# Optimization experiments

Measured on AMD Instinct MI355X. Metric: run time of the kernel, lower is better.

## Reference

```python
import jax, jax.numpy as jnp
import numpy as np
import math

N = 1024
C = 128
H = 4
HD = C // H  # 32
HID = C // 2  # geom_mlp hidden


def setup_inputs() -> dict:
    key = jax.random.key(0)
    ks = jax.random.split(key, 12)
    s = 0.02
    return {
        "x": jax.random.normal(ks[0], (N, C), jnp.float32),
        "y": jax.random.normal(ks[1], (N, C), jnp.float32),
        "pos": jax.random.normal(ks[2], (N, 3), jnp.float32),
        "Wq": jax.random.normal(ks[3], (C, C), jnp.float32) * s,
        "bq": jnp.zeros((C,), jnp.float32),
        "Wk": jax.random.normal(ks[4], (C, C), jnp.float32) * s,
        "bk": jnp.zeros((C,), jnp.float32),
        "Wv": jax.random.normal(ks[5], (C, C), jnp.float32) * s,
        "bv": jnp.zeros((C,), jnp.float32),
        "W1": jax.random.normal(ks[6], (3, HID), jnp.float32) * s,
        "b1": jnp.zeros((HID,), jnp.float32),
        "W2": jax.random.normal(ks[7], (HID, C), jnp.float32) * s,
        "b2": jnp.zeros((C,), jnp.float32),
    }


def _safe_norm(sq):
    # sqrt with zero (sub)gradient at 0, matching torch.norm behavior
    pos_mask = sq > 0
    return jnp.where(pos_mask, jnp.sqrt(jnp.where(pos_mask, sq, 1.0)), 0.0)


def reference(x, y, pos, Wq, bq, Wk, bk, Wv, bv, W1, b1, W2, b2):
    # pairwise geometry
    pos_diff = pos[:, None, :] - pos[None, :, :]          # [N, N, 3]
    dist = _safe_norm(jnp.sum(pos_diff * pos_diff, -1))   # [N, N]
    geom = jax.nn.relu(pos_diff @ W1 + b1) @ W2 + b2      # [N, N, C]
    geom = geom.reshape(N, N, H, HD)                      # per-head split

    q = (x @ Wq + bq).reshape(N, H, HD)
    k = (y @ Wk + bk).reshape(N, H, HD)
    v = (y @ Wv + bv).reshape(N, H, HD)

    attn = jnp.einsum("ihd,jhd->hij", q, k) / math.sqrt(HD)  # [H, N, N]
    geom_attn = jnp.einsum("ihd,ijhd->hij", q, geom)         # [H, N, N]
    scores = attn + geom_attn - dist[None, :, :]
    p = jax.nn.softmax(scores, axis=-1)
    out = jnp.einsum("hij,jhd->ihd", p, v).reshape(N, C)     # [N, C]
    return out
```

## Files before the change

kernel.cpp:

```cpp
#include <hip/hip_runtime.h>
#include <math.h>


typedef float v2f __attribute__((ext_vector_type(2)));
typedef float v4f __attribute__((ext_vector_type(4)));

#define L2E 1.4426950408889634f
#define RSL (0.17677669529663687f * L2E)

static __device__ __forceinline__ float dot4(float4 a, float4 b) {
  return a.x*b.x + a.y*b.y + a.z*b.z + a.w*b.w;
}
static __device__ __forceinline__ v2f fma2(v2f a, v2f b, v2f c) {
  return __builtin_elementwise_fma(a, b, c);
}
static __device__ __forceinline__ v4f fma4s(float s, v4f b, v4f c) {
  v4f sv = {s, s, s, s};
  return __builtin_elementwise_fma(sv, b, c);
}
static __device__ __forceinline__ unsigned int bfr(float f) {
  unsigned int b = __float_as_uint(f);
  return (b + 0x7fffu + ((b >> 16) & 1u)) >> 16;
}
static __device__ __forceinline__ unsigned int pack2(float lo, float hi) {
  return bfr(lo) | (bfr(hi) << 16);
}
static __device__ __forceinline__ v2f unpk(unsigned int a) {
  v2f r;
  r.x = __uint_as_float(a << 16);
  r.y = __uint_as_float(a & 0xffff0000u);
  return r;
}

__global__ __launch_bounds__(384) void k_pre(
    const float* __restrict__ x, const float* __restrict__ y, const float* __restrict__ pos,
    const float* __restrict__ Wq, const float* __restrict__ bq,
    const float* __restrict__ Wk, const float* __restrict__ bk,
    const float* __restrict__ Wv, const float* __restrict__ bv,
    const float* __restrict__ W1, const float* __restrict__ b1,
    const float* __restrict__ W2, const float* __restrict__ b2,
    float* __restrict__ q, float* __restrict__ v,
    unsigned int* __restrict__ kTb, unsigned int* __restrict__ uTb,
    float* __restrict__ sA, float* __restrict__ pos4w)
{
  __shared__ float xs[256], ys[256], qs[256];
  __shared__ __align__(16) float4 W2S[64*33];

  const int t  = threadIdx.x;
  const int n0 = blockIdx.x * 2;

  if (t < 256) { xs[t] = x[n0*128 + t]; ys[t] = y[n0*128 + t]; }
  {
    const float4* w2g = (const float4*)W2;
    #pragma unroll
    for (int r = 0; r < 6; ++r) {
      const int e = t + 384*r;
      if (e < 2048) W2S[(e>>5)*33 + (e&31)] = w2g[e];
    }
  }
  __syncthreads();

  {
    const int c   = t & 127;
    const int mat = t >> 7;
    const float* W    = (mat == 0) ? Wq : (mat == 1 ? Wk : Wv);
    const float* S    = (mat == 0) ? xs : ys;
    const float* bias = (mat == 0) ? bq : (mat == 1 ? bk : bv);
    float a0 = 0.f, a1 = 0.f;
    #pragma unroll 8
    for (int d = 0; d < 128; ++d) {
      const float w_ = W[d*128 + c];
      a0 = fmaf(S[d],       w_, a0);
      a1 = fmaf(S[128 + d], w_, a1);
    }
    const float bb = bias[c];
    a0 += bb; a1 += bb;
    if (mat == 0) {
      q[n0*128 + c] = a0 * RSL; q[(n0+1)*128 + c] = a1 * RSL;
      qs[c] = a0; qs[128 + c] = a1;
    } else if (mat == 2) {
      v[n0*128 + c] = a0; v[(n0+1)*128 + c] = a1;
    } else {
      const float b0 = __shfl_xor(a0, 1);
      const float b1 = __shfl_xor(a1, 1);
      if ((c & 1) == 0) {
        const int idx = ((c>>2)*1024)*2 + ((c>>1)&1);
        kTb[idx + (n0  )*2] = pack2(a0, b0);
        kTb[idx + (n0+1)*2] = pack2(a1, b1);
      }
    }
  }
  __syncthreads();

  if (t < 256) {
    const int m = t & 63, h = t >> 6;
    const float4* qs4 = (const float4*)qs;
    #pragma unroll
    for (int ii = 0; ii < 2; ++ii) {
      float acc = 0.f;
      #pragma unroll
      for (int ch = 0; ch < 8; ++ch)
        acc += dot4(qs4[ii*32 + h*8 + ch], W2S[m*33 + h*8 + ch]);
      sA[(n0+ii)*328 + 8 + (m>>2)*20 + h*4 + (m&3)] = acc * L2E;
    }
    if (t < 8) {
      const int ii = t >> 2, h2 = t & 3;
      float ca = 0.f;
      #pragma unroll
      for (int d = 0; d < 32; ++d) ca = fmaf(qs[ii*128 + h2*32 + d], b2[h2*32 + d], ca);
      sA[(n0+ii)*328 + h2] = ca * L2E;
    } else if (t < 16) {
      const int tt = t-8, ii = tt>>2, cc = tt&3;
      sA[(n0+ii)*328 + 4 + cc] = (cc < 3) ? pos[(n0+ii)*3 + cc] * L2E : 0.f;
    } else if (t < 24) {
      const int tt = t-16, ii = tt>>2, cc = tt&3;
      pos4w[(n0+ii)*4 + cc] = (cc < 3) ? pos[(n0+ii)*3 + cc] * L2E : 0.f;
    }
  } else if (t < 320) {
    const int tt = t - 256, ii = tt >> 5, mp = tt & 31;
    const int m0 = mp * 2;
    float ua0 = 0.f, ua1 = 0.f;
    #pragma unroll
    for (int cc = 0; cc < 3; ++cc) {
      const float p = pos[(n0+ii)*3 + cc];
      ua0 = fmaf(p, W1[cc*64 + m0    ], ua0);
      ua1 = fmaf(p, W1[cc*64 + m0 + 1], ua1);
    }
    sA[(n0+ii)*328 + 8 + (m0>>2)*20 + 16 + (m0&3)    ] = ua0 + b1[m0];
    sA[(n0+ii)*328 + 8 + (m0>>2)*20 + 16 + (m0&3) + 1] = ua1 + b1[m0+1];
    uTb[((mp>>1)*1024 + (n0+ii))*2 + (mp&1)] = pack2(ua0, ua1);
  }
}

__global__ __launch_bounds__(1024, 8) void k_attn(
    const float* __restrict__ q, const float* __restrict__ v,
    const uint2* __restrict__ kTb, const uint2* __restrict__ uTb,
    const float* __restrict__ sA, const v4f* __restrict__ pos4,
    float* __restrict__ out)
{
  __shared__ __align__(16) float eL[16*544];
  __shared__ __align__(16) float rnum[8192];
  __shared__ float rden[128];

  const int t     = threadIdx.x;
  const int i0    = blockIdx.x * 2;
  const int w     = t >> 6;
  const int lane  = t & 63;
  const int c4    = lane & 31;
  const int rep   = lane >> 5;
  const int hh    = c4 >> 3;

  const int jb = w*64;
  const int j  = jb + lane;

  const float* sA0 = sA + i0*328;
  const float* sA1 = sA0 + 328;
  const float* q0  = q + i0*128;
  const float* q1  = q0 + 128;

  const float c00 = sA0[0], c01 = sA0[1], c02 = sA0[2], c03 = sA0[3];
  const float c10 = sA1[0], c11 = sA1[1], c12 = sA1[2], c13 = sA1[3];
  const float p0x = sA0[4], p0y = sA0[5], p0z = sA0[6];
  const float p1x = sA1[4], p1y = sA1[5], p1z = sA1[6];

  const v4f pj = pos4[j];
  const float d0x = p0x-pj.x, d0y = p0y-pj.y, d0z = p0z-pj.z;
  const float d1x = p1x-pj.x, d1y = p1y-pj.y, d1z = p1z-pj.z;
  const float dist0 = sqrtf(d0x*d0x + d0y*d0y + d0z*d0z);
  const float dist1 = sqrtf(d1x*d1x + d1y*d1y + d1z*d1z);

  v2f g0a={0.f,0.f}, g0b={0.f,0.f}, g0c={0.f,0.f}, g0d={0.f,0.f};
  v2f g1a={0.f,0.f}, g1b={0.f,0.f}, g1c={0.f,0.f}, g1d={0.f,0.f};
  #pragma unroll 4
  for (int mb = 0; mb < 16; ++mb) {
    const uint2 up_ = uTb[mb*1024 + j];
    const v2f uj01 = unpk(up_.x), uj23 = unpk(up_.y);
    const v2f z = {0.f, 0.f};
    {
      const float* ab = sA0 + 8 + mb*20;
      const v2f h01 = __builtin_elementwise_max(*(const v2f*)(ab+16) - uj01, z);
      const v2f h23 = __builtin_elementwise_max(*(const v2f*)(ab+18) - uj23, z);
      g0a = fma2(h01, *(const v2f*)(ab+ 0), g0a); g0a = fma2(h23, *(const v2f*)(ab+ 2), g0a);
      g0b = fma2(h01, *(const v2f*)(ab+ 4), g0b); g0b = fma2(h23, *(const v2f*)(ab+ 6), g0b);
      g0c = fma2(h01, *(const v2f*)(ab+ 8), g0c); g0c = fma2(h23, *(const v2f*)(ab+10), g0c);
      g0d = fma2(h01, *(const v2f*)(ab+12), g0d); g0d = fma2(h23, *(const v2f*)(ab+14), g0d);
    }
    {
      const float* ab = sA1 + 8 + mb*20;
      const v2f h01 = __builtin_elementwise_max(*(const v2f*)(ab+16) - uj01, z);
      const v2f h23 = __builtin_elementwise_max(*(const v2f*)(ab+18) - uj23, z);
      g1a = fma2(h01, *(const v2f*)(ab+ 0), g1a); g1a = fma2(h23, *(const v2f*)(ab+ 2), g1a);
      g1b = fma2(h01, *(const v2f*)(ab+ 4), g1b); g1b = fma2(h23, *(const v2f*)(ab+ 6), g1b);
      g1c = fma2(h01, *(const v2f*)(ab+ 8), g1c); g1c = fma2(h23, *(const v2f*)(ab+10), g1c);
      g1d = fma2(h01, *(const v2f*)(ab+12), g1d); g1d = fma2(h23, *(const v2f*)(ab+14), g1d);
    }
  }

  v2f s0a={0.f,0.f}, s0b={0.f,0.f}, s0c={0.f,0.f}, s0d={0.f,0.f};
  v2f s1a={0.f,0.f}, s1b={0.f,0.f}, s1c={0.f,0.f}, s1d={0.f,0.f};
  #pragma unroll 8
  for (int cb = 0; cb < 8; ++cb) {
    const uint2 kp0 = kTb[(cb     )*1024 + j];
    const uint2 kp1 = kTb[(cb +  8)*1024 + j];
    const uint2 kp2 = kTb[(cb + 16)*1024 + j];
    const uint2 kp3 = kTb[(cb + 24)*1024 + j];
    const v2f k0a = unpk(kp0.x), k0b = unpk(kp0.y);
    const v2f k1a = unpk(kp1.x), k1b = unpk(kp1.y);
    const v2f k2a = unpk(kp2.x), k2b = unpk(kp2.y);
    const v2f k3a = unpk(kp3.x), k3b = unpk(kp3.y);
    s0a = fma2(k0a, *(const v2f*)(q0 + cb*4      ), s0a); s0a = fma2(k0b, *(const v2f*)(q0 + cb*4 +  2), s0a);
    s0b = fma2(k1a, *(const v2f*)(q0 + cb*4 + 32 ), s0b); s0b = fma2(k1b, *(const v2f*)(q0 + cb*4 + 34), s0b);
    s0c = fma2(k2a, *(const v2f*)(q0 + cb*4 + 64 ), s0c); s0c = fma2(k2b, *(const v2f*)(q0 + cb*4 + 66), s0c);
    s0d = fma2(k3a, *(const v2f*)(q0 + cb*4 + 96 ), s0d); s0d = fma2(k3b, *(const v2f*)(q0 + cb*4 + 98), s0d);
    s1a = fma2(k0a, *(const v2f*)(q1 + cb*4      ), s1a); s1a = fma2(k0b, *(const v2f*)(q1 + cb*4 +  2), s1a);
    s1b = fma2(k1a, *(const v2f*)(q1 + cb*4 + 32 ), s1b); s1b = fma2(k1b, *(const v2f*)(q1 + cb*4 + 34), s1b);
    s1c = fma2(k2a, *(const v2f*)(q1 + cb*4 + 64 ), s1c); s1c = fma2(k2b, *(const v2f*)(q1 + cb*4 + 66), s1c);
    s1d = fma2(k3a, *(const v2f*)(q1 + cb*4 + 96 ), s1d); s1d = fma2(k3b, *(const v2f*)(q1 + cb*4 + 98), s1d);
  }

  float lsum[8];
  float* eW = &eL[w*544];
  {
    const v2f t0a = s0a + g0a, t0b = s0b + g0b, t0c = s0c + g0c, t0d = s0d + g0d;
    const float p0 = exp2f(t0a.x + t0a.y + (c00 - dist0));
    const float p1 = exp2f(t0b.x + t0b.y + (c01 - dist0));
    const float p2 = exp2f(t0c.x + t0c.y + (c02 - dist0));
    const float p3 = exp2f(t0d.x + t0d.y + (c03 - dist0));
    lsum[0] = p0; lsum[1] = p1; lsum[2] = p2; lsum[3] = p3;
    eW[      lane] = p0; eW[ 68 + lane] = p1; eW[136 + lane] = p2; eW[204 + lane] = p3;
    const v2f t1a = s1a + g1a, t1b = s1b + g1b, t1c = s1c + g1c, t1d = s1d + g1d;
    const float r0 = exp2f(t1a.x + t1a.y + (c10 - dist1));
    const float r1 = exp2f(t1b.x + t1b.y + (c11 - dist1));
    const float r2 = exp2f(t1c.x + t1c.y + (c12 - dist1));
    const float r3 = exp2f(t1d.x + t1d.y + (c13 - dist1));
    lsum[4] = r0; lsum[5] = r1; lsum[6] = r2; lsum[7] = r3;
    eW[272 + lane] = r0; eW[340 + lane] = r1; eW[408 + lane] = r2; eW[476 + lane] = r3;
  }
  __builtin_amdgcn_wave_barrier();

  v4f acc0 = {0.f,0.f,0.f,0.f};
  v4f acc1 = {0.f,0.f,0.f,0.f};
  {
    const v4f* er0 = (const v4f*)&eL[w*544 +  hh    *68 + rep*32];
    const v4f* er1 = (const v4f*)&eL[w*544 + (4+hh) *68 + rep*32];
    const v4f* vg = (const v4f*)(v + jb*128);
    const int vbase = rep*32*32 + c4;
    #pragma unroll 4
    for (int jj4 = 0; jj4 < 8; ++jj4) {
      const v4f e0 = er0[jj4];
      const v4f e1 = er1[jj4];
      const v4f va = vg[vbase + (jj4*4+0)*32];
      const v4f vb = vg[vbase + (jj4*4+1)*32];
      const v4f vc = vg[vbase + (jj4*4+2)*32];
      const v4f vd = vg[vbase + (jj4*4+3)*32];
      acc0 = fma4s(e0.x, va, acc0); acc1 = fma4s(e1.x, va, acc1);
      acc0 = fma4s(e0.y, vb, acc0); acc1 = fma4s(e1.y, vb, acc1);
      acc0 = fma4s(e0.z, vc, acc0); acc1 = fma4s(e1.z, vc, acc1);
      acc0 = fma4s(e0.w, vd, acc0); acc1 = fma4s(e1.w, vd, acc1);
    }
  }
  __builtin_amdgcn_wave_barrier();

  #pragma unroll
  for (int mm = 1; mm < 64; mm <<= 1) {
    #pragma unroll
    for (int r8 = 0; r8 < 8; ++r8) lsum[r8] += __shfl_xor(lsum[r8], mm);
  }
  ((v4f*)rnum)[((w*2+0)*2 + rep)*32 + c4] = acc0;
  ((v4f*)rnum)[((w*2+1)*2 + rep)*32 + c4] = acc1;
  if (lane == 0) {
    #pragma unroll
    for (int r8 = 0; r8 < 8; ++r8) rden[w*8 + r8] = lsum[r8];
  }
  __syncthreads();

  if (t < 256) {
    const int ii = t >> 7, c = t & 127;
    float num = 0.f, den = 0.f;
    #pragma unroll
    for (int ww = 0; ww < 16; ++ww) {
      num += rnum[((ww*2+ii)*2+0)*128 + c];
      num += rnum[((ww*2+ii)*2+1)*128 + c];
      den += rden[ww*8 + ii*4 + (c>>5)];
    }
    out[(i0+ii)*128 + c] = num / den;
  }
}

extern "C" void kernel_launch(void* const* d_in, const int* in_sizes, int n_in,
                              void* d_out, int out_size, void* d_ws, size_t ws_size,
                              hipStream_t stream) {
  const float* x   = (const float*)d_in[0];
  const float* y   = (const float*)d_in[1];
  const float* pos = (const float*)d_in[2];
  const float* Wq  = (const float*)d_in[3];
  const float* bq  = (const float*)d_in[4];
  const float* Wk  = (const float*)d_in[5];
  const float* bk  = (const float*)d_in[6];
  const float* Wv  = (const float*)d_in[7];
  const float* bv  = (const float*)d_in[8];
  const float* W1  = (const float*)d_in[9];
  const float* b1  = (const float*)d_in[10];
  const float* W2  = (const float*)d_in[11];
  const float* b2  = (const float*)d_in[12];

  float* ws = (float*)d_ws;
  float*        q    = ws;
  float*        v    = ws + 131072;
  unsigned int* kTb  = (unsigned int*)(ws + 262144);
  unsigned int* uTb  = (unsigned int*)(ws + 327680);
  float*        sA   = ws + 360448;
  float*        pos4 = ws + 696320;
  float*        out  = (float*)d_out;

  k_pre<<<dim3(512), dim3(384), 0, stream>>>(x, y, pos, Wq, bq, Wk, bk, Wv, bv,
                                             W1, b1, W2, b2,
                                             q, v, kTb, uTb, sA, pos4);
  k_attn<<<dim3(512), dim3(1024), 0, stream>>>(q, v, (const uint2*)kTb,
                                               (const uint2*)uTb, sA,
                                               (const v4f*)pos4, out);
}
```

Before: 116.9 us.

## Switch QK and PV products to packed fp16 dot2 with fp16 q/k/v storage

Stores scaled q, k and v as packed fp16 pairs (k moves from bf16 to fp16, v is laid out j-pair interleaved) and computes QK scores and the P·V accumulation with v_dot2 fp16 instructions instead of fp32 FMAs. The softmax numerators are rounded to fp16 so the row sums match the values used in the weighted sum. The denominator reduction is moved ahead of the PV loop. This halves the q/v global traffic and the FMA count, at the cost of fp16 range and precision risk on scores and exponentials.

```diff
diff --git a/kernel.cpp b/kernel.cpp
--- a/kernel.cpp
+++ b/kernel.cpp
@@ -1,9 +1,11 @@
 #include <hip/hip_runtime.h>
+#include <hip/hip_fp16.h>
 #include <math.h>
 
 
 typedef float v2f __attribute__((ext_vector_type(2)));
 typedef float v4f __attribute__((ext_vector_type(4)));
+typedef __fp16 h2f __attribute__((ext_vector_type(2)));
 
 #define L2E 1.4426950408889634f
 #define RSL (0.17677669529663687f * L2E)
@@ -13,10 +15,6 @@
 }
 static __device__ __forceinline__ v2f fma2(v2f a, v2f b, v2f c) {
   return __builtin_elementwise_fma(a, b, c);
-}
-static __device__ __forceinline__ v4f fma4s(float s, v4f b, v4f c) {
-  v4f sv = {s, s, s, s};
-  return __builtin_elementwise_fma(sv, b, c);
 }
 static __device__ __forceinline__ unsigned int bfr(float f) {
   unsigned int b = __float_as_uint(f);
@@ -30,6 +28,23 @@
   r.x = __uint_as_float(a << 16);
   r.y = __uint_as_float(a & 0xffff0000u);
   return r;
+}
+static __device__ __forceinline__ unsigned int pkh(float lo, float hi) {
+  h2f r = __builtin_amdgcn_cvt_pkrtz(lo, hi);
+  return __builtin_bit_cast(unsigned int, r);
+}
+static __device__ __forceinline__ unsigned int pkrn(float lo, float hi) {
+  unsigned int a = (unsigned int)__half_as_ushort(__float2half(lo));
+  unsigned int b = (unsigned int)__half_as_ushort(__float2half(hi));
+  return a | (b << 16);
+}
+static __device__ __forceinline__ float fdot2h(unsigned int a_, unsigned int b_, float acc) {
+  return __builtin_amdgcn_fdot2(__builtin_bit_cast(h2f, a_),
+                                __builtin_bit_cast(h2f, b_), acc, false);
+}
+static __device__ __forceinline__ float r2hf(float x) {
+  h2f t = __builtin_amdgcn_cvt_pkrtz(x, x);
+  return (float)t.x;
 }
 
 __global__ __launch_bounds__(384) void k_pre(
@@ -39,7 +54,7 @@
     const float* __restrict__ Wv, const float* __restrict__ bv,
     const float* __restrict__ W1, const float* __restrict__ b1,
     const float* __restrict__ W2, const float* __restrict__ b2,
-    float* __restrict__ q, float* __restrict__ v,
+    unsigned int* __restrict__ qT, unsigned int* __restrict__ vJ,
     unsigned int* __restrict__ kTb, unsigned int* __restrict__ uTb,
     float* __restrict__ sA, float* __restrict__ pos4w)
 {
@@ -76,17 +91,23 @@
     const float bb = bias[c];
     a0 += bb; a1 += bb;
     if (mat == 0) {
-      q[n0*128 + c] = a0 * RSL; q[(n0+1)*128 + c] = a1 * RSL;
       qs[c] = a0; qs[128 + c] = a1;
+      const float sa0 = a0 * RSL, sa1 = a1 * RSL;
+      const float tb0 = __shfl_xor(sa0, 1);
+      const float tb1 = __shfl_xor(sa1, 1);
+      if ((c & 1) == 0) {
+        qT[(n0  )*64 + (c>>1)] = pkh(sa0, tb0);
+        qT[(n0+1)*64 + (c>>1)] = pkh(sa1, tb1);
+      }
     } else if (mat == 2) {
-      v[n0*128 + c] = a0; v[(n0+1)*128 + c] = a1;
+      vJ[(n0>>1)*128 + c] = pkrn(a0, a1);
     } else {
       const float b0 = __shfl_xor(a0, 1);
       const float b1 = __shfl_xor(a1, 1);
       if ((c & 1) == 0) {
         const int idx = ((c>>2)*1024)*2 + ((c>>1)&1);
-        kTb[idx + (n0  )*2] = pack2(a0, b0);
-        kTb[idx + (n0+1)*2] = pack2(a1, b1);
+        kTb[idx + (n0  )*2] = pkh(a0, b0);
+        kTb[idx + (n0+1)*2] = pkh(a1, b1);
       }
     }
   }
@@ -133,7 +154,7 @@
 }
 
 __global__ __launch_bounds__(1024, 8) void k_attn(
-    const float* __restrict__ q, const float* __restrict__ v,
+    const unsigned int* __restrict__ qT, const unsigned int* __restrict__ vJ,
     const uint2* __restrict__ kTb, const uint2* __restrict__ uTb,
     const float* __restrict__ sA, const v4f* __restrict__ pos4,
     float* __restrict__ out)
@@ -155,8 +176,6 @@
 
   const float* sA0 = sA + i0*328;
   const float* sA1 = sA0 + 328;
-  const float* q0  = q + i0*128;
-  const float* q1  = q0 + 128;
 
   const float c00 = sA0[0], c01 = sA0[1], c02 = sA0[2], c03 = sA0[3];
   const float c10 = sA1[0], c11 = sA1[1], c12 = sA1[2], c13 = sA1[3];
@@ -196,82 +215,80 @@
     }
   }
 
-  v2f s0a={0.f,0.f}, s0b={0.f,0.f}, s0c={0.f,0.f}, s0d={0.f,0.f};
-  v2f s1a={0.f,0.f}, s1b={0.f,0.f}, s1c={0.f,0.f}, s1d={0.f,0.f};
-  #pragma unroll 8
-  for (int cb = 0; cb < 8; ++cb) {
-    const uint2 kp0 = kTb[(cb     )*1024 + j];
-    const uint2 kp1 = kTb[(cb +  8)*1024 + j];
-    const uint2 kp2 = kTb[(cb + 16)*1024 + j];
-    const uint2 kp3 = kTb[(cb + 24)*1024 + j];
-    const v2f k0a = unpk(kp0.x), k0b = unpk(kp0.y);
-    const v2f k1a = unpk(kp1.x), k1b = unpk(kp1.y);
-    const v2f k2a = unpk(kp2.x), k2b = unpk(kp2.y);
-    const v2f k3a = unpk(kp3.x), k3b = unpk(kp3.y);
-    s0a = fma2(k0a, *(const v2f*)(q0 + cb*4      ), s0a); s0a = fma2(k0b, *(const v2f*)(q0 + cb*4 +  2), s0a);
-    s0b = fma2(k1a, *(const v2f*)(q0 + cb*4 + 32 ), s0b); s0b = fma2(k1b, *(const v2f*)(q0 + cb*4 + 34), s0b);
-    s0c = fma2(k2a, *(const v2f*)(q0 + cb*4 + 64 ), s0c); s0c = fma2(k2b, *(const v2f*)(q0 + cb*4 + 66), s0c);
-    s0d = fma2(k3a, *(const v2f*)(q0 + cb*4 + 96 ), s0d); s0d = fma2(k3b, *(const v2f*)(q0 + cb*4 + 98), s0d);
-    s1a = fma2(k0a, *(const v2f*)(q1 + cb*4      ), s1a); s1a = fma2(k0b, *(const v2f*)(q1 + cb*4 +  2), s1a);
-    s1b = fma2(k1a, *(const v2f*)(q1 + cb*4 + 32 ), s1b); s1b = fma2(k1b, *(const v2f*)(q1 + cb*4 + 34), s1b);
-    s1c = fma2(k2a, *(const v2f*)(q1 + cb*4 + 64 ), s1c); s1c = fma2(k2b, *(const v2f*)(q1 + cb*4 + 66), s1c);
-    s1d = fma2(k3a, *(const v2f*)(q1 + cb*4 + 96 ), s1d); s1d = fma2(k3b, *(const v2f*)(q1 + cb*4 + 98), s1d);
+  float t0a = g0a.x + g0a.y, t0b = g0b.x + g0b.y;
+  float t0c = g0c.x + g0c.y, t0d = g0d.x + g0d.y;
+  float t1a = g1a.x + g1a.y, t1b = g1b.x + g1b.y;
+  float t1c = g1c.x + g1c.y, t1d = g1d.x + g1d.y;
+
+  {
+    const unsigned int* qT0 = qT + i0*64;
+    const unsigned int* qT1 = qT0 + 64;
+    #pragma unroll 8
+    for (int cb = 0; cb < 8; ++cb) {
+      const uint2 kp0 = kTb[(cb     )*1024 + j];
+      const uint2 kp1 = kTb[(cb +  8)*1024 + j];
+      const uint2 kp2 = kTb[(cb + 16)*1024 + j];
+      const uint2 kp3 = kTb[(cb + 24)*1024 + j];
+      t0a = fdot2h(kp0.x, qT0[     cb*2], t0a); t0a = fdot2h(kp0.y, qT0[     cb*2+1], t0a);
+      t0b = fdot2h(kp1.x, qT0[16 + cb*2], t0b); t0b = fdot2h(kp1.y, qT0[16 + cb*2+1], t0b);
+      t0c = fdot2h(kp2.x, qT0[32 + cb*2], t0c); t0c = fdot2h(kp2.y, qT0[32 + cb*2+1], t0c);
+      t0d = fdot2h(kp3.x, qT0[48 + cb*2], t0d); t0d = fdot2h(kp3.y, qT0[48 + cb*2+1], t0d);
+      t1a = fdot2h(kp0.x, qT1[     cb*2], t1a); t1a = fdot2h(kp0.y, qT1[     cb*2+1], t1a);
+      t1b = fdot2h(kp1.x, qT1[16 + cb*2], t1b); t1b = fdot2h(kp1.y, qT1[16 + cb*2+1], t1b);
+      t1c = fdot2h(kp2.x, qT1[32 + cb*2], t1c); t1c = fdot2h(kp2.y, qT1[32 + cb*2+1], t1c);
+      t1d = fdot2h(kp3.x, qT1[48 + cb*2], t1d); t1d = fdot2h(kp3.y, qT1[48 + cb*2+1], t1d);
+    }
   }
 
   float lsum[8];
   float* eW = &eL[w*544];
   {
-    const v2f t0a = s0a + g0a, t0b = s0b + g0b, t0c = s0c + g0c, t0d = s0d + g0d;
-    const float p0 = exp2f(t0a.x + t0a.y + (c00 - dist0));
-    const float p1 = exp2f(t0b.x + t0b.y + (c01 - dist0));
-    const float p2 = exp2f(t0c.x + t0c.y + (c02 - dist0));
-    const float p3 = exp2f(t0d.x + t0d.y + (c03 - dist0));
+    const float p0 = r2hf(exp2f(t0a + (c00 - dist0)));
+    const float p1 = r2hf(exp2f(t0b + (c01 - dist0)));
+    const float p2 = r2hf(exp2f(t0c + (c02 - dist0)));
+    const float p3 = r2hf(exp2f(t0d + (c03 - dist0)));
     lsum[0] = p0; lsum[1] = p1; lsum[2] = p2; lsum[3] = p3;
     eW[      lane] = p0; eW[ 68 + lane] = p1; eW[136 + lane] = p2; eW[204 + lane] = p3;
-    const v2f t1a = s1a + g1a, t1b = s1b + g1b, t1c = s1c + g1c, t1d = s1d + g1d;
-    const float r0 = exp2f(t1a.x + t1a.y + (c10 - dist1));
-    const float r1 = exp2f(t1b.x + t1b.y + (c11 - dist1));
-    const float r2 = exp2f(t1c.x + t1c.y + (c12 - dist1));
-    const float r3 = exp2f(t1d.x + t1d.y + (c13 - dist1));
+    const float r0 = r2hf(exp2f(t1a + (c10 - dist1)));
+    const float r1 = r2hf(exp2f(t1b + (c11 - dist1)));
+    const float r2 = r2hf(exp2f(t1c + (c12 - dist1)));
+    const float r3 = r2hf(exp2f(t1d + (c13 - dist1)));
     lsum[4] = r0; lsum[5] = r1; lsum[6] = r2; lsum[7] = r3;
     eW[272 + lane] = r0; eW[340 + lane] = r1; eW[408 + lane] = r2; eW[476 + lane] = r3;
   }
   __builtin_amdgcn_wave_barrier();
 
+  #pragma unroll
+  for (int mm = 1; mm < 64; mm <<= 1) {
+    #pragma unroll
+    for (int r8 = 0; r8 < 8; ++r8) lsum[r8] += __shfl_xor(lsum[r8], mm);
+  }
+  if (lane == 0) {
+    #pragma unroll
+    for (int r8 = 0; r8 < 8; ++r8) rden[w*8 + r8] = lsum[r8];
+  }
+
   v4f acc0 = {0.f,0.f,0.f,0.f};
   v4f acc1 = {0.f,0.f,0.f,0.f};
   {
-    const v4f* er0 = (const v4f*)&eL[w*544 +  hh    *68 + rep*32];
-    const v4f* er1 = (const v4f*)&eL[w*544 + (4+hh) *68 + rep*32];
-    const v4f* vg = (const v4f*)(v + jb*128);
-    const int vbase = rep*32*32 + c4;
+    const float* er0 = &eL[w*544 +  hh   *68 + rep*32];
+    const float* er1 = &eL[w*544 + (4+hh)*68 + rep*32];
+    const uint4* vg = (const uint4*)vJ + (w*32 + rep*16)*32 + c4;
     #pragma unroll 4
-    for (int jj4 = 0; jj4 < 8; ++jj4) {
-      const v4f e0 = er0[jj4];
-      const v4f e1 = er1[jj4];
-      const v4f va = vg[vbase + (jj4*4+0)*32];
-      const v4f vb = vg[vbase + (jj4*4+1)*32];
-      const v4f vc = vg[vbase + (jj4*4+2)*32];
-      const v4f vd = vg[vbase + (jj4*4+3)*32];
-      acc0 = fma4s(e0.x, va, acc0); acc1 = fma4s(e1.x, va, acc1);
-      acc0 = fma4s(e0.y, vb, acc0); acc1 = fma4s(e1.y, vb, acc1);
-      acc0 = fma4s(e0.z, vc, acc0); acc1 = fma4s(e1.z, vc, acc1);
-      acc0 = fma4s(e0.w, vd, acc0); acc1 = fma4s(e1.w, vd, acc1);
+    for (int m = 0; m < 16; ++m) {
+      const uint4 vw = vg[m*32];
+      const unsigned int e0 = pkh(er0[2*m], er0[2*m+1]);
+      const unsigned int e1 = pkh(er1[2*m], er1[2*m+1]);
+      acc0.x = fdot2h(vw.x, e0, acc0.x); acc0.y = fdot2h(vw.y, e0, acc0.y);
+      acc0.z = fdot2h(vw.z, e0, acc0.z); acc0.w = fdot2h(vw.w, e0, acc0.w);
+      acc1.x = fdot2h(vw.x, e1, acc1.x); acc1.y = fdot2h(vw.y, e1, acc1.y);
+      acc1.z = fdot2h(vw.z, e1, acc1.z); acc1.w = fdot2h(vw.w, e1, acc1.w);
     }
   }
   __builtin_amdgcn_wave_barrier();
 
-  #pragma unroll
-  for (int mm = 1; mm < 64; mm <<= 1) {
-    #pragma unroll
-    for (int r8 = 0; r8 < 8; ++r8) lsum[r8] += __shfl_xor(lsum[r8], mm);
-  }
   ((v4f*)rnum)[((w*2+0)*2 + rep)*32 + c4] = acc0;
   ((v4f*)rnum)[((w*2+1)*2 + rep)*32 + c4] = acc1;
-  if (lane == 0) {
-    #pragma unroll
-    for (int r8 = 0; r8 < 8; ++r8) rden[w*8 + r8] = lsum[r8];
-  }
   __syncthreads();
 
   if (t < 256) {
@@ -305,8 +322,8 @@
   const float* b2  = (const float*)d_in[12];
 
   float* ws = (float*)d_ws;
-  float*        q    = ws;
-  float*        v    = ws + 131072;
+  unsigned int* qT   = (unsigned int*)ws;
+  unsigned int* vJ   = (unsigned int*)(ws + 131072);
   unsigned int* kTb  = (unsigned int*)(ws + 262144);
   unsigned int* uTb  = (unsigned int*)(ws + 327680);
   float*        sA   = ws + 360448;
@@ -315,8 +332,8 @@
 
   k_pre<<<dim3(512), dim3(384), 0, stream>>>(x, y, pos, Wq, bq, Wk, bk, Wv, bv,
                                              W1, b1, W2, b2,
-                                             q, v, kTb, uTb, sA, pos4);
-  k_attn<<<dim3(512), dim3(1024), 0, stream>>>(q, v, (const uint2*)kTb,
+                                             qT, vJ, kTb, uTb, sA, pos4);
+  k_attn<<<dim3(512), dim3(1024), 0, stream>>>(qT, vJ, (const uint2*)kTb,
                                                (const uint2*)uTb, sA,
                                                (const v4f*)pos4, out);
 }
```

Result: faster. 114.1 us (-2.4%).
